# Kernel optimization log

Measured on AMD Instinct MI355X. Metric: run time of the kernel, lower is better.

## Reference

```python
import jax, jax.numpy as jnp
import numpy as np

DIM = 1024; HEADS = 16; HEAD = 64; FFN_H = 4096
LE = 8; TOPK = 2; DIM_E = 512; DIM_S = 1024
B = 1; S = 2048; N = B * S; NMOE = 2
THETA = 10000.0; EPS = 1e-6; RSF = 1.0


def rmsnorm(x, g):
    return x * jax.lax.rsqrt(jnp.mean(x * x, axis=-1, keepdims=True) + EPS) * g


def rotary(x):
    # x: [b, h, s, a]; matches RotaryEmb: split halves, y1=x1*cos+x2*sin, y2=-x1*sin+x2*cos
    a = x.shape[-1]; s = x.shape[2]
    inv_freq = (1.0 / THETA) ** (jnp.arange(0, a, 2, dtype=jnp.float32) / a)
    freqs = jnp.arange(s, dtype=jnp.float32)[:, None] * inv_freq[None, :]  # [s, a/2]
    cos, sin = jnp.cos(freqs), jnp.sin(freqs)
    x1, x2 = jnp.split(x, 2, axis=-1)
    return jnp.concatenate([x1 * cos + x2 * sin, -x1 * sin + x2 * cos], axis=-1)


def attention(x, attn_w, attn_o, doc):
    # causal + same-document masked attention (flex_attention mask_mod equivalent)
    b, s, d = x.shape
    xq, xk, xv = jnp.split(x @ attn_w, 3, axis=-1)
    def heads(t):
        return t.reshape(b, s, HEADS, HEAD).transpose(0, 2, 1, 3)
    xq, xk, xv = heads(xq), heads(xk), heads(xv)
    xq, xk = rotary(xq), rotary(xk)
    scores = jnp.einsum('bhqa,bhka->bhqk', xq, xk) / jnp.sqrt(jnp.float32(HEAD))
    q_idx = jnp.arange(s)
    mask = (q_idx[:, None] >= q_idx[None, :])[None] & (doc[:, :, None] == doc[:, None, :])
    scores = jnp.where(mask[:, None, :, :], scores, -jnp.inf)
    probs = jax.nn.softmax(scores, axis=-1)
    out = jnp.einsum('bhqk,bhka->bhqa', probs, xv)
    return out.transpose(0, 2, 1, 3).reshape(b, s, d) @ attn_o


def dense_layer(x, aw, ao, up, down, ag, fg, doc):
    xi = attention(rmsnorm(x, ag), aw, ao, doc) + x
    xf = rmsnorm(xi, fg)
    x1, x2 = jnp.split(xf @ up, 2, axis=-1)
    return (jax.nn.silu(x1) * x2) @ down + xi


def moe_layer(x, aw, ao, ag, fg, experts, tkeys, rbias, sup, sdown, idx, vals, doc):
    xi = attention(rmsnorm(x, ag), aw, ao, doc) + x
    xf = rmsnorm(xi, fg)                     # [b,s,d]
    flat = xf.reshape(-1, DIM)               # [N,d]
    # routing: base values + token-key logits + bias, sigmoid, renormalize
    tv = flat @ tkeys                        # [N,le]
    vals = vals + jnp.take_along_axis(tv, idx, axis=-1) + rbias[idx]
    sc = jax.nn.sigmoid(vals)
    sc = sc / jnp.sum(sc, axis=-1, keepdims=True) * RSF   # [N,k]
    # grouped-gemm experts (SwiGLU per expert); dense-over-experts then gather
    h1 = jnp.einsum('nd,edh->neh', flat, experts[0])
    h2 = jnp.einsum('nd,edh->neh', flat, experts[1])
    y_all = jnp.einsum('neh,edh->ned', jax.nn.silu(h1) * h2, experts[2])
    y_sel = jnp.take_along_axis(y_all, idx[:, :, None], axis=1)   # [N,k,d]
    y = jnp.sum(y_sel * sc[:, :, None], axis=1).reshape(xf.shape)
    # shared expert
    x1, x2 = jnp.split(xf @ sup, 2, axis=-1)
    y = y + (jax.nn.silu(x1) * x2) @ sdown
    return y + xi


def setup_inputs() -> dict:
    key = jax.random.key(0)
    ks = jax.random.split(key, 24)
    w = lambda k, shp: (jax.random.normal(k, shp, dtype=jnp.float32) * 0.02)
    inp = {
        'x': jax.random.normal(ks[0], (B, S, DIM), dtype=jnp.float32),
        'doc': jnp.sort(jax.random.randint(ks[1], (B, S), 0, 4), axis=-1).astype(jnp.int32),
        'indices': jax.random.randint(ks[2], (NMOE, N, TOPK), 0, LE).astype(jnp.int64),
        'values': jax.random.normal(ks[3], (NMOE, N, TOPK), dtype=jnp.float32),
        # 2 dense layers (first_k=1, last_k=1)
        'dense_attn_w': w(ks[4], (2, DIM, 3 * DIM)),
        'dense_attn_o': w(ks[5], (2, DIM, DIM)),
        'dense_ffn_up': w(ks[6], (2, DIM, 2 * FFN_H)),
        'dense_ffn_down': w(ks[7], (2, FFN_H, DIM)),
        'dense_attn_g': jnp.ones((2, DIM), dtype=jnp.float32),
        'dense_ffn_g': jnp.ones((2, DIM), dtype=jnp.float32),
        # 2 MoE layers
        'moe_attn_w': w(ks[8], (NMOE, DIM, 3 * DIM)),
        'moe_attn_o': w(ks[9], (NMOE, DIM, DIM)),
        'moe_attn_g': jnp.ones((NMOE, DIM), dtype=jnp.float32),
        'moe_ffn_g': jnp.ones((NMOE, DIM), dtype=jnp.float32),
        'moe_experts': w(ks[10], (NMOE, 3, LE, DIM, DIM_E)),
        'moe_token_keys': w(ks[11], (NMOE, DIM, LE)),
        'moe_router_bias': jnp.zeros((NMOE, LE), dtype=jnp.float32),
        'moe_shared_up': w(ks[12], (NMOE, DIM, 2 * DIM_S)),
        'moe_shared_down': w(ks[13], (NMOE, DIM_S, DIM)),
    }
    return inp


def reference(x, doc, indices, values, dense_attn_w, dense_attn_o, dense_ffn_up,
              dense_ffn_down, dense_attn_g, dense_ffn_g, moe_attn_w, moe_attn_o,
              moe_attn_g, moe_ffn_g, moe_experts, moe_token_keys, moe_router_bias,
              moe_shared_up, moe_shared_down):
    x = dense_layer(x, dense_attn_w[0], dense_attn_o[0], dense_ffn_up[0],
                    dense_ffn_down[0], dense_attn_g[0], dense_ffn_g[0], doc)
    for i in range(NMOE):
        x = moe_layer(x, moe_attn_w[i], moe_attn_o[i], moe_attn_g[i], moe_ffn_g[i],
                      moe_experts[i], moe_token_keys[i], moe_router_bias[i],
                      moe_shared_up[i], moe_shared_down[i], indices[i], values[i], doc)
    x = dense_layer(x, dense_attn_w[1], dense_attn_o[1], dense_ffn_up[1],
                    dense_ffn_down[1], dense_attn_g[1], dense_ffn_g[1], doc)
    return x
```

## Files before the change

### kernel.cpp

```cpp
#include <hip/hip_runtime.h>
#include <cmath>
#include <cstddef>
#include <cstdint>

#define DIMM   1024
#define HEADS  16
#define HEADD  64
#define FFN_H  4096
#define LE     8
#define TOPK   2
#define DIM_E  512
#define DIM_S  1024
#define NTOK   2048

typedef __bf16 bf16x8 __attribute__((ext_vector_type(8)));
typedef float  f32x4  __attribute__((ext_vector_type(4)));

union BF4 { __bf16 h[4]; uint2 u; };
union BF2 { __bf16 h[2]; uint32_t u; };

__device__ __forceinline__ void ldg_lds16(const __bf16* g, __bf16* l) {
    __builtin_amdgcn_global_load_lds(
        (const __attribute__((address_space(1))) uint32_t*)g,
        (__attribute__((address_space(3))) uint32_t*)l, 16, 0, 0);
}

__global__ __launch_bounds__(256) void rmsnorm_bf(
    const float* __restrict__ x, const float* __restrict__ g,
    __bf16* __restrict__ y)
{
    const int row = blockIdx.x;
    const int t = threadIdx.x;
    const float* xr = x + (size_t)row * DIMM;
    float4 v = *(const float4*)(xr + t * 4);
    float ss = v.x * v.x + v.y * v.y + v.z * v.z + v.w * v.w;
    #pragma unroll
    for (int off = 32; off > 0; off >>= 1) ss += __shfl_down(ss, off, 64);
    __shared__ float ws[4];
    if ((t & 63) == 0) ws[t >> 6] = ss;
    __syncthreads();
    const float tot = ws[0] + ws[1] + ws[2] + ws[3];
    const float scale = rsqrtf(tot * (1.0f / DIMM) + 1e-6f);
    const float4 gv = *(const float4*)(g + t * 4);
    BF4 o;
    o.h[0] = (__bf16)(v.x * scale * gv.x);
    o.h[1] = (__bf16)(v.y * scale * gv.y);
    o.h[2] = (__bf16)(v.z * scale * gv.z);
    o.h[3] = (__bf16)(v.w * scale * gv.w);
    *(uint2*)(y + (size_t)row * DIMM + t * 4) = o.u;
}

template <typename OutT>
__global__ __launch_bounds__(256) void gemm_bf_t(
    const __bf16* __restrict__ A, const __bf16* __restrict__ BT,
    const float* __restrict__ add, OutT* __restrict__ C,
    int M, int N, int K)
{
    __shared__ __bf16 As[128 * 32];
    __shared__ __bf16 Bs[128 * 32];
    const int t = threadIdx.x;
    const int m0 = blockIdx.y * 128, n0 = blockIdx.x * 128;
    const int lane = t & 63;
    const int wv = t >> 6;
    const int mw = (wv >> 1) * 64, nw = (wv & 1) * 64;
    const int fr = lane & 15;
    const int fk = ((lane >> 4) ^ ((fr >> 1) & 3)) * 8;
    const int r0 = t >> 2;
    const int q0l = (t & 3) * 8;
    const int q0s = ((t & 3) ^ ((t >> 3) & 3)) * 8;

    const __bf16* gA0 = A + (size_t)(m0 + r0) * K + q0s;
    const __bf16* gA1 = A + (size_t)(m0 + 64 + r0) * K + q0s;
    const __bf16* gB0 = BT + (size_t)(n0 + r0) * K + q0s;
    const __bf16* gB1 = BT + (size_t)(n0 + 64 + r0) * K + q0s;
    __bf16* lA0 = &As[r0 * 32 + q0l];
    __bf16* lA1 = &As[(64 + r0) * 32 + q0l];
    __bf16* lB0 = &Bs[r0 * 32 + q0l];
    __bf16* lB1 = &Bs[(64 + r0) * 32 + q0l];

    f32x4 acc[4][4];
    #pragma unroll
    for (int i = 0; i < 4; ++i)
        #pragma unroll
        for (int j = 0; j < 4; ++j) acc[i][j] = (f32x4){0.f, 0.f, 0.f, 0.f};

    for (int k0 = 0; k0 < K; k0 += 32) {
        __syncthreads();
        ldg_lds16(gA0 + k0, lA0);
        ldg_lds16(gA1 + k0, lA1);
        ldg_lds16(gB0 + k0, lB0);
        ldg_lds16(gB1 + k0, lB1);
        __syncthreads();
        bf16x8 af[4], bfr[4];
        #pragma unroll
        for (int i = 0; i < 4; ++i) {
            af[i]  = *(const bf16x8*)&As[(mw + i * 16 + fr) * 32 + fk];
            bfr[i] = *(const bf16x8*)&Bs[(nw + i * 16 + fr) * 32 + fk];
        }
        #pragma unroll
        for (int i = 0; i < 4; ++i)
            #pragma unroll
            for (int j = 0; j < 4; ++j)
                acc[i][j] = __builtin_amdgcn_mfma_f32_16x16x32_bf16(
                    af[i], bfr[j], acc[i][j], 0, 0, 0);
    }
    const int cn = lane & 15, cr = (lane >> 4) * 4;
    #pragma unroll
    for (int i = 0; i < 4; ++i)
        #pragma unroll
        for (int j = 0; j < 4; ++j)
            #pragma unroll
            for (int r = 0; r < 4; ++r) {
                const size_t off = (size_t)(m0 + mw + i * 16 + cr + r) * N
                                 + (n0 + nw + j * 16 + cn);
                if constexpr (__is_same(OutT, float))
                    C[off] = acc[i][j][r] + (add ? add[off] : 0.f);
                else
                    C[off] = (__bf16)acc[i][j][r];
            }
}

__global__ __launch_bounds__(256) void gemm_bf_splitk(
    const __bf16* __restrict__ A, const __bf16* __restrict__ BT,
    float* __restrict__ P, int M, int N, int K, int KS)
{
    __shared__ __bf16 As[128 * 32];
    __shared__ __bf16 Bs[128 * 32];
    const int t = threadIdx.x;
    const int m0 = blockIdx.y * 128, n0 = blockIdx.x * 128;
    const int kz0 = blockIdx.z * KS;
    const int lane = t & 63;
    const int wv = t >> 6;
    const int mw = (wv >> 1) * 64, nw = (wv & 1) * 64;
    const int fr = lane & 15;
    const int fk = ((lane >> 4) ^ ((fr >> 1) & 3)) * 8;
    const int r0 = t >> 2;
    const int q0l = (t & 3) * 8;
    const int q0s = ((t & 3) ^ ((t >> 3) & 3)) * 8;

    const __bf16* gA0 = A + (size_t)(m0 + r0) * K + q0s;
    const __bf16* gA1 = A + (size_t)(m0 + 64 + r0) * K + q0s;
    const __bf16* gB0 = BT + (size_t)(n0 + r0) * K + q0s;
    const __bf16* gB1 = BT + (size_t)(n0 + 64 + r0) * K + q0s;
    __bf16* lA0 = &As[r0 * 32 + q0l];
    __bf16* lA1 = &As[(64 + r0) * 32 + q0l];
    __bf16* lB0 = &Bs[r0 * 32 + q0l];
    __bf16* lB1 = &Bs[(64 + r0) * 32 + q0l];

    f32x4 acc[4][4];
    #pragma unroll
    for (int i = 0; i < 4; ++i)
        #pragma unroll
        for (int j = 0; j < 4; ++j) acc[i][j] = (f32x4){0.f, 0.f, 0.f, 0.f};

    for (int k0 = kz0; k0 < kz0 + KS; k0 += 32) {
        __syncthreads();
        ldg_lds16(gA0 + k0, lA0);
        ldg_lds16(gA1 + k0, lA1);
        ldg_lds16(gB0 + k0, lB0);
        ldg_lds16(gB1 + k0, lB1);
        __syncthreads();
        bf16x8 af[4], bfr[4];
        #pragma unroll
        for (int i = 0; i < 4; ++i) {
            af[i]  = *(const bf16x8*)&As[(mw + i * 16 + fr) * 32 + fk];
            bfr[i] = *(const bf16x8*)&Bs[(nw + i * 16 + fr) * 32 + fk];
        }
        #pragma unroll
        for (int i = 0; i < 4; ++i)
            #pragma unroll
            for (int j = 0; j < 4; ++j)
                acc[i][j] = __builtin_amdgcn_mfma_f32_16x16x32_bf16(
                    af[i], bfr[j], acc[i][j], 0, 0, 0);
    }
    float* Pz = P + (size_t)blockIdx.z * M * N;
    const int cn = lane & 15, cr = (lane >> 4) * 4;
    #pragma unroll
    for (int i = 0; i < 4; ++i)
        #pragma unroll
        for (int j = 0; j < 4; ++j)
            #pragma unroll
            for (int r = 0; r < 4; ++r) {
                const size_t off = (size_t)(m0 + mw + i * 16 + cr + r) * N
                                 + (n0 + nw + j * 16 + cn);
                Pz[off] = acc[i][j][r];
            }
}

__global__ __launch_bounds__(256) void gemm_glu(
    const __bf16* __restrict__ A, const __bf16* __restrict__ BT,
    const float* __restrict__ sc, __bf16* __restrict__ G,
    int M, int Nout, int K, int pairOff)
{
    __shared__ __bf16 As[128 * 32];
    __shared__ __bf16 Bs[128 * 32];
    const int t = threadIdx.x;
    const int m0 = blockIdx.y * 128;
    const int b  = blockIdx.x;
    const int lane = t & 63;
    const int wv = t >> 6;
    const int mw = (wv >> 1) * 64, nw = (wv & 1) * 64;
    const int fr = lane & 15;
    const int fk = ((lane >> 4) ^ ((fr >> 1) & 3)) * 8;
    const int r0 = t >> 2;
    const int q0l = (t & 3) * 8;
    const int q0s = ((t & 3) ^ ((t >> 3) & 3)) * 8;

    const int grow0 = b * 64 + ((r0 >> 6) ? 32 : 0) + (r0 & 31)
                    + ((r0 >> 5) & 1) * pairOff;
    const int grow1 = grow0 + 32;

    const __bf16* gA0 = A + (size_t)(m0 + r0) * K + q0s;
    const __bf16* gA1 = A + (size_t)(m0 + 64 + r0) * K + q0s;
    const __bf16* gB0 = BT + (size_t)grow0 * K + q0s;
    const __bf16* gB1 = BT + (size_t)grow1 * K + q0s;
    __bf16* lA0 = &As[r0 * 32 + q0l];
    __bf16* lA1 = &As[(64 + r0) * 32 + q0l];
    __bf16* lB0 = &Bs[r0 * 32 + q0l];
    __bf16* lB1 = &Bs[(64 + r0) * 32 + q0l];

    f32x4 acc[4][4];
    #pragma unroll
    for (int i = 0; i < 4; ++i)
        #pragma unroll
        for (int j = 0; j < 4; ++j) acc[i][j] = (f32x4){0.f, 0.f, 0.f, 0.f};

    for (int k0 = 0; k0 < K; k0 += 32) {
        __syncthreads();
        ldg_lds16(gA0 + k0, lA0);
        ldg_lds16(gA1 + k0, lA1);
        ldg_lds16(gB0 + k0, lB0);
        ldg_lds16(gB1 + k0, lB1);
        __syncthreads();
        bf16x8 af[4], bfr[4];
        #pragma unroll
        for (int i = 0; i < 4; ++i) {
            af[i]  = *(const bf16x8*)&As[(mw + i * 16 + fr) * 32 + fk];
            bfr[i] = *(const bf16x8*)&Bs[(nw + i * 16 + fr) * 32 + fk];
        }
        #pragma unroll
        for (int i = 0; i < 4; ++i)
            #pragma unroll
            for (int j = 0; j < 4; ++j)
                acc[i][j] = __builtin_amdgcn_mfma_f32_16x16x32_bf16(
                    af[i], bfr[j], acc[i][j], 0, 0, 0);
    }
    const int cn = lane & 15, cr = (lane >> 4) * 4;
    const int e = (b * 64) >> 9;
    #pragma unroll
    for (int i = 0; i < 4; ++i)
        #pragma unroll
        for (int r = 0; r < 4; ++r) {
            const int m = m0 + mw + i * 16 + cr + r;
            const float s = sc ? sc[m * LE + e] : 1.f;
            #pragma unroll
            for (int j = 0; j < 2; ++j) {
                const float h1 = acc[i][j][r];
                const float h2 = acc[i][j + 2][r];
                const float o = (h1 / (1.f + __expf(-h1))) * h2 * s;
                const int col = b * 64 + (nw >> 1) + j * 16 + cn;
                G[(size_t)m * Nout + col] = (__bf16)o;
            }
        }
}

__global__ __launch_bounds__(512, 2) void gemm_glu256(
    const __bf16* __restrict__ A, const __bf16* __restrict__ BT,
    const float* __restrict__ sc, __bf16* __restrict__ G,
    int M, int Nout, int K, int pairOff)
{
    __shared__ __bf16 As[4][256 * 32];
    __shared__ __bf16 Bs[4][256 * 32];
    const int t = threadIdx.x;
    const int m0 = blockIdx.y * 256;
    const int b  = blockIdx.x;
    const int lane = t & 63;
    const int wv = t >> 6;
    const int wr = wv >> 2, wc = wv & 3;
    const int fr = lane & 15;
    const int fk = ((lane >> 4) ^ ((fr >> 1) & 3)) * 8;

    const int r0 = t >> 2;
    const int c  = t & 3;
    const int cs = (c ^ ((r0 >> 1) & 3)) * 8;
    const int ldst = r0 * 32 + c * 8;

    const int rem0 = r0 & 63;
    const int grow0 = b * 128 + (r0 >> 6) * 32 + ((rem0 >> 4) & 1) * 16
                    + (rem0 & 15) + (rem0 >> 5) * pairOff;
    const int r1 = r0 + 128;
    const int rem1 = r1 & 63;
    const int grow1 = b * 128 + (r1 >> 6) * 32 + ((rem1 >> 4) & 1) * 16
                    + (rem1 & 15) + (rem1 >> 5) * pairOff;

    const __bf16* gA0 = A + (size_t)(m0 + r0) * K + cs;
    const __bf16* gA1 = A + (size_t)(m0 + 128 + r0) * K + cs;
    const __bf16* gB0 = BT + (size_t)grow0 * K + cs;
    const __bf16* gB1 = BT + (size_t)grow1 * K + cs;

    const int NT = K >> 5;

#define STAGE256(bi, kt) do {                                   \
        const int _k = (kt) << 5;                               \
        ldg_lds16(gA0 + _k, &As[bi][ldst]);                     \
        ldg_lds16(gA1 + _k, &As[bi][128 * 32 + ldst]);          \
        ldg_lds16(gB0 + _k, &Bs[bi][ldst]);                     \
        ldg_lds16(gB1 + _k, &Bs[bi][128 * 32 + ldst]);          \
    } while (0)

    f32x4 acc[8][4];
    #pragma unroll
    for (int i = 0; i < 8; ++i)
        #pragma unroll
        for (int j = 0; j < 4; ++j) acc[i][j] = (f32x4){0.f, 0.f, 0.f, 0.f};

    STAGE256(0, 0);
    STAGE256(1, 1);
    STAGE256(2, 2);
    asm volatile("s_waitcnt vmcnt(8)" ::: "memory");
    __builtin_amdgcn_s_barrier();
    asm volatile("" ::: "memory");

    for (int kt = 0; kt < NT; ++kt) {
        const int bi = kt & 3;
        if (kt + 3 < NT) STAGE256((kt + 3) & 3, kt + 3);

        bf16x8 af[8], bf[4];
        const __bf16* Ab = &As[bi][(wr * 128 + fr) * 32 + fk];
        #pragma unroll
        for (int i = 0; i < 8; ++i) af[i] = *(const bf16x8*)(Ab + i * 16 * 32);
        const __bf16* Bb = &Bs[bi][(wc * 64 + fr) * 32 + fk];
        #pragma unroll
        for (int j = 0; j < 4; ++j) bf[j] = *(const bf16x8*)(Bb + j * 16 * 32);

        #pragma unroll
        for (int i = 0; i < 8; ++i)
            #pragma unroll
            for (int j = 0; j < 4; ++j)
                acc[i][j] = __builtin_amdgcn_mfma_f32_16x16x32_bf16(
                    af[i], bf[j], acc[i][j], 0, 0, 0);

        if (kt < NT - 1) {
            if (kt < NT - 3)       asm volatile("s_waitcnt vmcnt(8)" ::: "memory");
            else if (kt == NT - 3) asm volatile("s_waitcnt vmcnt(4)" ::: "memory");
            else                   asm volatile("s_waitcnt vmcnt(0)" ::: "memory");
            __builtin_amdgcn_s_barrier();
            asm volatile("" ::: "memory");
        }
    }
#undef STAGE256

    const int cn = lane & 15, cr = (lane >> 4) * 4;
    const int e = b >> 2;
    #pragma unroll
    for (int i = 0; i < 8; ++i)
        #pragma unroll
        for (int r = 0; r < 4; ++r) {
            const int m = m0 + wr * 128 + i * 16 + cr + r;
            const float s = sc ? sc[m * LE + e] : 1.f;
            #pragma unroll
            for (int j = 0; j < 2; ++j) {
                const float h1 = acc[i][j][r];
                const float h2 = acc[i][j + 2][r];
                const float o = (h1 / (1.f + __expf(-h1))) * h2 * s;
                const int col = b * 128 + wc * 32 + j * 16 + cn;
                G[(size_t)m * Nout + col] = (__bf16)o;
            }
        }
}

__global__ __launch_bounds__(256) void reduce4_add(
    const float* __restrict__ P, const float* __restrict__ add,
    float* __restrict__ out, size_t MN)
{
    const size_t i = ((size_t)blockIdx.x * 256 + threadIdx.x) * 4;
    float4 s  = *(const float4*)(P + i);
    const float4 s1 = *(const float4*)(P + MN + i);
    const float4 s2 = *(const float4*)(P + 2 * MN + i);
    const float4 s3 = *(const float4*)(P + 3 * MN + i);
    const float4 a  = *(const float4*)(add + i);
    s.x += s1.x + s2.x + s3.x + a.x;
    s.y += s1.y + s2.y + s3.y + a.y;
    s.z += s1.z + s2.z + s3.z + a.z;
    s.w += s1.w + s2.w + s3.w + a.w;
    *(float4*)(out + i) = s;
}

__global__ __launch_bounds__(256) void reduce2_add(
    const float* __restrict__ P, const float* __restrict__ add,
    float* __restrict__ out, size_t MN)
{
    const size_t i = ((size_t)blockIdx.x * 256 + threadIdx.x) * 4;
    float4 s  = *(const float4*)(P + i);
    const float4 s1 = *(const float4*)(P + MN + i);
    const float4 a  = *(const float4*)(add + i);
    s.x += s1.x + a.x;
    s.y += s1.y + a.y;
    s.z += s1.z + a.z;
    s.w += s1.w + a.w;
    *(float4*)(out + i) = s;
}

__global__ __launch_bounds__(256) void transpose_cast(
    const float* __restrict__ in, __bf16* __restrict__ out, int R, int C)
{
    __shared__ float tile[32][33];
    const int bx = blockIdx.x * 32, by = blockIdx.y * 32;
    const size_t bz = (size_t)blockIdx.z * R * C;
    const int tx = threadIdx.x & 31, ty = threadIdx.x >> 5;
    const float* ip = in + bz;
    __bf16* op = out + bz;
    #pragma unroll
    for (int i = 0; i < 4; ++i)
        tile[ty + i * 8][tx] = ip[(size_t)(by + ty + i * 8) * C + bx + tx];
    __syncthreads();
    #pragma unroll
    for (int i = 0; i < 4; ++i)
        op[(size_t)(bx + ty + i * 8) * R + by + tx] = (__bf16)tile[tx][ty + i * 8];
}

__global__ __launch_bounds__(256) void cast_w2(
    const float* __restrict__ in, __bf16* __restrict__ out)
{
    const int i = blockIdx.x * 256 + threadIdx.x;
    const int d = i >> 12, r = i & 4095;
    const int e = r >> 9, h = r & 511;
    out[i] = (__bf16)in[(size_t)e * (DIMM * DIM_E) + d * DIM_E + h];
}

__global__ __launch_bounds__(256) void rotary_kernel(float* __restrict__ qkv)
{
    const int i = blockIdx.x * 256 + threadIdx.x;
    const int s = i >> 9;
    const int rem = i & 511;
    const int h = rem >> 5;
    const int j = rem & 31;
    const float inv_freq = __expf(-(float)j * (9.210340371976184f / 32.f));
    const float f = (float)s * inv_freq;
    float sn, cs;
    sincosf(f, &sn, &cs);
    float* base = qkv + (size_t)s * 3072 + h * 64 + j;
    const float q1 = base[0], q2 = base[32];
    base[0]  = q1 * cs + q2 * sn;
    base[32] = -q1 * sn + q2 * cs;
    const float k1 = base[1024], k2 = base[1024 + 32];
    base[1024]      = k1 * cs + k2 * sn;
    base[1024 + 32] = -k1 * sn + k2 * cs;
}

#define KS_STRIDE 72
#define VT_STRIDE 72
#define PW_STRIDE 36
#define LOG2E 1.4426950408889634f

__global__ __launch_bounds__(256) void attn_mfma(
    const float* __restrict__ qkv, const int* __restrict__ doc,
    __bf16* __restrict__ out)
{
    const int h = blockIdx.x;
    const int qb = blockIdx.y;
    const int t = threadIdx.x;
    const int wv = t >> 6, lane = t & 63;
    const int l15 = lane & 15, lhi = lane >> 4;
    const int q0w = qb * 64 + wv * 16;

    __shared__ __bf16 Ks[64 * KS_STRIDE];
    __shared__ __bf16 Vt[64 * VT_STRIDE];
    __shared__ float  Pw[4][16 * PW_STRIDE];
    __shared__ int    docs[64];

    bf16x8 qf[2];
    {
        const float* qrow = qkv + (size_t)(q0w + l15) * 3072 + h * 64 + lhi * 8;
        #pragma unroll
        for (int db = 0; db < 2; ++db) {
            const float4 v0 = *(const float4*)(qrow + db * 32);
            const float4 v1 = *(const float4*)(qrow + db * 32 + 4);
            bf16x8 f;
            f[0] = (__bf16)(v0.x * 0.125f); f[1] = (__bf16)(v0.y * 0.125f);
            f[2] = (__bf16)(v0.z * 0.125f); f[3] = (__bf16)(v0.w * 0.125f);
            f[4] = (__bf16)(v1.x * 0.125f); f[5] = (__bf16)(v1.y * 0.125f);
            f[6] = (__bf16)(v1.z * 0.125f); f[7] = (__bf16)(v1.w * 0.125f);
            qf[db] = f;
        }
    }
    int myDoc[4];
    #pragma unroll
    for (int rg = 0; rg < 4; ++rg) myDoc[rg] = doc[q0w + lhi * 4 + rg];

    float mrow[4] = {-INFINITY, -INFINITY, -INFINITY, -INFINITY};
    float lrow[4] = {0.f, 0.f, 0.f, 0.f};
    f32x4 oacc[4];
    #pragma unroll
    for (int nb = 0; nb < 4; ++nb) oacc[nb] = (f32x4){0.f, 0.f, 0.f, 0.f};

    const int docQ0 = doc[qb * 64];
    const int ntiles = qb + 1;

    for (int kt = 0; kt < ntiles; ++kt) {
        if (doc[kt * 64 + 63] < docQ0) continue;
        __syncthreads();
        {
            const int key = t >> 2, dof = (t & 3) * 16;
            const float* kr = qkv + (size_t)(kt * 64 + key) * 3072 + 1024 + h * 64 + dof;
            float kv[16];
            *(float4*)&kv[0]  = *(const float4*)(kr + 0);
            *(float4*)&kv[4]  = *(const float4*)(kr + 4);
            *(float4*)&kv[8]  = *(const float4*)(kr + 8);
            *(float4*)&kv[12] = *(const float4*)(kr + 12);
            bf16x8 p0, p1;
            #pragma unroll
            for (int j = 0; j < 8; ++j) { p0[j] = (__bf16)kv[j]; p1[j] = (__bf16)kv[8 + j]; }
            *(bf16x8*)&Ks[key * KS_STRIDE + dof] = p0;
            *(bf16x8*)&Ks[key * KS_STRIDE + dof + 8] = p1;
            const int k2 = (t & 31) * 2, df = (t >> 5) * 8;
            const float* vr0 = qkv + (size_t)(kt * 64 + k2) * 3072 + 2048 + h * 64 + df;
            float va[8], vb[8];
            *(float4*)&va[0] = *(const float4*)(vr0 + 0);
            *(float4*)&va[4] = *(const float4*)(vr0 + 4);
            *(float4*)&vb[0] = *(const float4*)(vr0 + 3072);
            *(float4*)&vb[4] = *(const float4*)(vr0 + 3076);
            #pragma unroll
            for (int d = 0; d < 8; ++d) {
                BF2 wpk;
                wpk.h[0] = (__bf16)va[d];
                wpk.h[1] = (__bf16)vb[d];
                *(uint32_t*)&Vt[(df + d) * VT_STRIDE + k2] = wpk.u;
            }
            if (t < 64) docs[t] = doc[kt * 64 + t];
        }
        __syncthreads();

        #pragma unroll
        for (int g = 0; g < 2; ++g) {
            f32x4 s[2];
            #pragma unroll
            for (int sg = 0; sg < 2; ++sg) {
                const int keyloc = g * 32 + sg * 16;
                const bf16x8 kf0 = *(const bf16x8*)&Ks[(keyloc + l15) * KS_STRIDE + lhi * 8];
                const bf16x8 kf1 = *(const bf16x8*)&Ks[(keyloc + l15) * KS_STRIDE + 32 + lhi * 8];
                f32x4 a = (f32x4){0.f, 0.f, 0.f, 0.f};
                a = __builtin_amdgcn_mfma_f32_16x16x32_bf16(qf[0], kf0, a, 0, 0, 0);
                a = __builtin_amdgcn_mfma_f32_16x16x32_bf16(qf[1], kf1, a, 0, 0, 0);
                s[sg] = a;
            }
            float sv0[4], sv1[4], cmax[4];
            #pragma unroll
            for (int rg = 0; rg < 4; ++rg) {
                const int r = q0w + lhi * 4 + rg;
                const int key0 = kt * 64 + g * 32 + l15;
                const bool v0 = (key0 <= r) && (docs[g * 32 + l15] == myDoc[rg]);
                const bool v1 = (key0 + 16 <= r) && (docs[g * 32 + 16 + l15] == myDoc[rg]);
                sv0[rg] = v0 ? s[0][rg] : -INFINITY;
                sv1[rg] = v1 ? s[1][rg] : -INFINITY;
                cmax[rg] = fmaxf(sv0[rg], sv1[rg]);
            }
            #pragma unroll
            for (int off = 1; off < 16; off <<= 1)
                #pragma unroll
                for (int rg = 0; rg < 4; ++rg)
                    cmax[rg] = fmaxf(cmax[rg], __shfl_xor(cmax[rg], off, 64));
            float alpha[4], p0[4], p1[4], rsum[4];
            #pragma unroll
            for (int rg = 0; rg < 4; ++rg) {
                const float mn = fmaxf(mrow[rg], cmax[rg]);
                alpha[rg] = (mn == -INFINITY) ? 1.f : exp2f((mrow[rg] - mn) * LOG2E);
                p0[rg] = (sv0[rg] == -INFINITY) ? 0.f : exp2f((sv0[rg] - mn) * LOG2E);
                p1[rg] = (sv1[rg] == -INFINITY) ? 0.f : exp2f((sv1[rg] - mn) * LOG2E);
                rsum[rg] = p0[rg] + p1[rg];
                mrow[rg] = mn;
            }
            #pragma unroll
            for (int off = 1; off < 16; off <<= 1)
                #pragma unroll
                for (int rg = 0; rg < 4; ++rg)
                    rsum[rg] += __shfl_xor(rsum[rg], off, 64);
            #pragma unroll
            for (int rg = 0; rg < 4; ++rg)
                lrow[rg] = lrow[rg] * alpha[rg] + rsum[rg];
            #pragma unroll
            for (int nb = 0; nb < 4; ++nb)
                #pragma unroll
                for (int rg = 0; rg < 4; ++rg)
                    oacc[nb][rg] *= alpha[rg];
            float* pp = &Pw[wv][0];
            #pragma unroll
            for (int rg = 0; rg < 4; ++rg) {
                pp[(lhi * 4 + rg) * PW_STRIDE + l15] = p0[rg];
                pp[(lhi * 4 + rg) * PW_STRIDE + 16 + l15] = p1[rg];
            }
            const f32x4 pa = *(const f32x4*)&pp[l15 * PW_STRIDE + lhi * 8];
            const f32x4 pb = *(const f32x4*)&pp[l15 * PW_STRIDE + lhi * 8 + 4];
            bf16x8 pf;
            pf[0] = (__bf16)pa[0]; pf[1] = (__bf16)pa[1];
            pf[2] = (__bf16)pa[2]; pf[3] = (__bf16)pa[3];
            pf[4] = (__bf16)pb[0]; pf[5] = (__bf16)pb[1];
            pf[6] = (__bf16)pb[2]; pf[7] = (__bf16)pb[3];
            #pragma unroll
            for (int nb = 0; nb < 4; ++nb) {
                const bf16x8 vf = *(const bf16x8*)&Vt[(nb * 16 + l15) * VT_STRIDE + g * 32 + lhi * 8];
                oacc[nb] = __builtin_amdgcn_mfma_f32_16x16x32_bf16(pf, vf, oacc[nb], 0, 0, 0);
            }
        }
    }
    float inv[4];
    #pragma unroll
    for (int rg = 0; rg < 4; ++rg) inv[rg] = 1.f / lrow[rg];
    #pragma unroll
    for (int nb = 0; nb < 4; ++nb)
        #pragma unroll
        for (int rg = 0; rg < 4; ++rg)
            out[(size_t)(q0w + lhi * 4 + rg) * DIMM + h * 64 + nb * 16 + l15] =
                (__bf16)(oacc[nb][rg] * inv[rg]);
}

__global__ __launch_bounds__(64) void router_bf(
    const __bf16* __restrict__ xf, const float* __restrict__ tkeys,
    const float* __restrict__ rbias, const int* __restrict__ idx,
    const float* __restrict__ vals, float* __restrict__ sc)
{
    const int n = blockIdx.x;
    const int t = threadIdx.x;
    const int e0 = idx[n * 2 + 0], e1 = idx[n * 2 + 1];
    float a0 = 0.f, a1 = 0.f;
    for (int d = t; d < DIMM; d += 64) {
        const float xv = (float)xf[(size_t)n * DIMM + d];
        a0 += xv * tkeys[d * LE + e0];
        a1 += xv * tkeys[d * LE + e1];
    }
    #pragma unroll
    for (int off = 32; off > 0; off >>= 1) {
        a0 += __shfl_down(a0, off, 64);
        a1 += __shfl_down(a1, off, 64);
    }
    if (t == 0) {
        const float v0 = vals[n * 2 + 0] + a0 + rbias[e0];
        const float v1 = vals[n * 2 + 1] + a1 + rbias[e1];
        const float s0 = 1.f / (1.f + __expf(-v0));
        const float s1 = 1.f / (1.f + __expf(-v1));
        const float inv = 1.f / (s0 + s1);
        float r[LE];
        #pragma unroll
        for (int e = 0; e < LE; ++e) r[e] = 0.f;
        r[e0] += s0 * inv;
        r[e1] += s1 * inv;
        #pragma unroll
        for (int e = 0; e < LE; ++e) sc[n * LE + e] = r[e];
    }
}

struct Scratch {
    float *qkv, *xi, *t1, *sc, *xA, *xB, *part;
    __bf16 *xn_bf, *attnO_bf, *xf_bf, *wbuf, *gact_bf, *gs_bf;
};

static void attn_block(const float* x_in, const __bf16* awT, const __bf16* aoT,
                       const float* ag, const int* doc, Scratch& w, hipStream_t s)
{
    rmsnorm_bf<<<NTOK, 256, 0, s>>>(x_in, ag, w.xn_bf);
    gemm_bf_t<float><<<dim3(24, 16), 256, 0, s>>>(w.xn_bf, awT, nullptr, w.qkv, NTOK, 3072, 1024);
    rotary_kernel<<<(NTOK * 512) / 256, 256, 0, s>>>(w.qkv);
    attn_mfma<<<dim3(HEADS, NTOK / 64), 256, 0, s>>>(w.qkv, doc, w.attnO_bf);
    gemm_bf_splitk<<<dim3(8, 16, 2), 256, 0, s>>>(w.attnO_bf, aoT, w.qkv, NTOK, 1024, 1024, 512);
    reduce2_add<<<(NTOK * 1024) / 1024, 256, 0, s>>>(w.qkv, x_in, w.xi, (size_t)NTOK * 1024);
}

static void dense_layer_run(const float* x_in, float* x_out,
                            const float* aw, const float* ao,
                            const float* up, const float* down,
                            const float* ag, const float* fg,
                            const int* doc, Scratch& w, hipStream_t s)
{
    __bf16* awT = w.wbuf;
    __bf16* aoT = w.wbuf + 3145728;
    __bf16* upT = w.wbuf + 4194304;
    __bf16* dnT = w.wbuf + 12582912;
    transpose_cast<<<dim3(96, 32, 1), 256, 0, s>>>(aw, awT, 1024, 3072);
    transpose_cast<<<dim3(32, 32, 1), 256, 0, s>>>(ao, aoT, 1024, 1024);
    transpose_cast<<<dim3(256, 32, 1), 256, 0, s>>>(up, upT, 1024, 8192);
    transpose_cast<<<dim3(32, 128, 1), 256, 0, s>>>(down, dnT, 4096, 1024);
    attn_block(x_in, awT, aoT, ag, doc, w, s);
    rmsnorm_bf<<<NTOK, 256, 0, s>>>(w.xi, fg, w.xf_bf);
    gemm_glu256<<<dim3(32, 8), 512, 0, s>>>(w.xf_bf, upT, nullptr, w.gact_bf, NTOK, 4096, 1024, 4096);
    gemm_bf_splitk<<<dim3(8, 16, 4), 256, 0, s>>>(w.gact_bf, dnT, w.part, NTOK, 1024, 4096, 1024);
    reduce4_add<<<(NTOK * 1024) / 1024, 256, 0, s>>>(w.part, w.xi, x_out, (size_t)NTOK * 1024);
}

static void moe_layer_run(const float* x_in, float* x_out,
                          const float* aw, const float* ao,
                          const float* ag, const float* fg,
                          const float* experts, const float* tkeys,
                          const float* rbias, const float* sup,
                          const float* sdn, const int* idx, const float* vals,
                          const int* doc, Scratch& w, hipStream_t s)
{
    __bf16* awT  = w.wbuf;
    __bf16* aoT  = w.wbuf + 3145728;
    __bf16* w01T = w.wbuf + 4194304;
    __bf16* w2c  = w.wbuf + 12582912;
    __bf16* supT = w.wbuf + 16777216;
    __bf16* sdnT = w.wbuf + 18874368;
    const size_t EW = (size_t)LE * DIMM * DIM_E;
    transpose_cast<<<dim3(96, 32, 1), 256, 0, s>>>(aw, awT, 1024, 3072);
    transpose_cast<<<dim3(32, 32, 1), 256, 0, s>>>(ao, aoT, 1024, 1024);
    transpose_cast<<<dim3(16, 32, 8), 256, 0, s>>>(experts, w01T, 1024, 512);
    transpose_cast<<<dim3(16, 32, 8), 256, 0, s>>>(experts + EW, w01T + 4194304, 1024, 512);
    cast_w2<<<16384, 256, 0, s>>>(experts + 2 * EW, w2c);
    transpose_cast<<<dim3(64, 32, 1), 256, 0, s>>>(sup, supT, 1024, 2048);
    transpose_cast<<<dim3(32, 32, 1), 256, 0, s>>>(sdn, sdnT, 1024, 1024);

    attn_block(x_in, awT, aoT, ag, doc, w, s);
    rmsnorm_bf<<<NTOK, 256, 0, s>>>(w.xi, fg, w.xf_bf);
    router_bf<<<NTOK, 64, 0, s>>>(w.xf_bf, tkeys, rbias, idx, vals, w.sc);
    gemm_glu256<<<dim3(32, 8), 512, 0, s>>>(w.xf_bf, w01T, w.sc, w.gact_bf, NTOK, 4096, 1024, 4096);
    gemm_glu<<<dim3(16, 16), 256, 0, s>>>(w.xf_bf, supT, nullptr, w.gs_bf, NTOK, 1024, 1024, 1024);
    gemm_bf_splitk<<<dim3(8, 16, 2), 256, 0, s>>>(w.gs_bf, sdnT, w.part, NTOK, 1024, 1024, 512);
    reduce2_add<<<(NTOK * 1024) / 1024, 256, 0, s>>>(w.part, w.xi, w.t1, (size_t)NTOK * 1024);
    gemm_bf_splitk<<<dim3(8, 16, 4), 256, 0, s>>>(w.gact_bf, w2c, w.part, NTOK, 1024, 4096, 1024);
    reduce4_add<<<(NTOK * 1024) / 1024, 256, 0, s>>>(w.part, w.t1, x_out, (size_t)NTOK * 1024);
}

extern "C" void kernel_launch(void* const* d_in, const int* in_sizes, int n_in,
                              void* d_out, int out_size, void* d_ws, size_t ws_size,
                              hipStream_t stream)
{
    (void)in_sizes; (void)n_in; (void)out_size; (void)ws_size;
    const float* x       = (const float*)d_in[0];
    const int*   doc     = (const int*)d_in[1];
    const int*   indices = (const int*)d_in[2];
    const float* values  = (const float*)d_in[3];
    const float* d_aw    = (const float*)d_in[4];
    const float* d_ao    = (const float*)d_in[5];
    const float* d_up    = (const float*)d_in[6];
    const float* d_down  = (const float*)d_in[7];
    const float* d_ag    = (const float*)d_in[8];
    const float* d_fg    = (const float*)d_in[9];
    const float* m_aw    = (const float*)d_in[10];
    const float* m_ao    = (const float*)d_in[11];
    const float* m_ag    = (const float*)d_in[12];
    const float* m_fg    = (const float*)d_in[13];
    const float* m_ex    = (const float*)d_in[14];
    const float* m_tk    = (const float*)d_in[15];
    const float* m_rb    = (const float*)d_in[16];
    const float* m_sup   = (const float*)d_in[17];
    const float* m_sdn   = (const float*)d_in[18];

    Scratch w;
    float* f = (float*)d_ws;
    w.qkv = f; f += 6291456;
    w.xi  = f; f += 2097152;
    float* h12 = f; f += 16777216;
    w.t1  = h12 + 8388608;
    w.sc  = f; f += 16384;
    w.xA  = f; f += 2097152;
    w.xB  = f; f += 2097152;
    __bf16* b = (__bf16*)f;
    w.xn_bf    = b; b += 2097152;
    w.attnO_bf = b; b += 2097152;
    w.xf_bf    = b; b += 2097152;
    w.wbuf     = b; b += 19922944;
    w.gact_bf  = (__bf16*)w.qkv;
    w.gs_bf    = (__bf16*)w.qkv + 8388608;
    w.part     = h12;

    float* out = (float*)d_out;

    dense_layer_run(x, w.xA, d_aw, d_ao, d_up, d_down, d_ag, d_fg, doc, w, stream);
    const size_t EXL = (size_t)3 * LE * DIMM * DIM_E;
    moe_layer_run(w.xA, w.xB,
                  m_aw, m_ao, m_ag, m_fg,
                  m_ex, m_tk, m_rb, m_sup, m_sdn,
                  indices, values, doc, w, stream);
    moe_layer_run(w.xB, w.xA,
                  m_aw + (size_t)DIMM * 3 * DIMM, m_ao + (size_t)DIMM * DIMM,
                  m_ag + DIMM, m_fg + DIMM,
                  m_ex + EXL, m_tk + DIMM * LE, m_rb + LE,
                  m_sup + (size_t)DIMM * 2 * DIM_S, m_sdn + (size_t)DIM_S * DIMM,
                  indices + (size_t)NTOK * TOPK, values + (size_t)NTOK * TOPK,
                  doc, w, stream);
    dense_layer_run(w.xA, out,
                    d_aw + (size_t)DIMM * 3 * DIMM, d_ao + (size_t)DIMM * DIMM,
                    d_up + (size_t)DIMM * 2 * FFN_H, d_down + (size_t)FFN_H * DIMM,
                    d_ag + DIMM, d_fg + DIMM, doc, w, stream);
}
```

Before: 1.296 ms.

## Fuse rotary and q-scaling into QKV GEMM epilogue with bf16 output

The QKV projection GEMM now applies rotary embedding and the 1/sqrt(d) query scaling in its epilogue and writes bf16 instead of fp32, which removes the separate rotary kernel. The attention kernel reads bf16 Q/K/V directly, loads K tiles into LDS asynchronously with an XOR swizzle instead of converting fp32 in registers, and drops the padded K stride. This targets the fp32 round trips and an extra kernel launch, at the cost of computing sincos in the GEMM epilogue and rounding Q/K/V to bf16 slightly earlier.

```diff
diff --git a/kernel.cpp b/kernel.cpp
--- a/kernel.cpp
+++ b/kernel.cpp
@@ -120,6 +120,94 @@
             }
 }
 
+__global__ __launch_bounds__(256) void gemm_qkv_rot(
+    const __bf16* __restrict__ A, const __bf16* __restrict__ BT,
+    __bf16* __restrict__ C, int M, int N, int K)
+{
+    __shared__ __bf16 As[128 * 32];
+    __shared__ __bf16 Bs[128 * 32];
+    const int t = threadIdx.x;
+    const int m0 = blockIdx.y * 128, n0 = blockIdx.x * 128;
+    const int lane = t & 63;
+    const int wv = t >> 6;
+    const int mw = (wv >> 1) * 64, nw = (wv & 1) * 64;
+    const int fr = lane & 15;
+    const int fk = ((lane >> 4) ^ ((fr >> 1) & 3)) * 8;
+    const int r0 = t >> 2;
+    const int q0l = (t & 3) * 8;
+    const int q0s = ((t & 3) ^ ((t >> 3) & 3)) * 8;
+
+    const __bf16* gA0 = A + (size_t)(m0 + r0) * K + q0s;
+    const __bf16* gA1 = A + (size_t)(m0 + 64 + r0) * K + q0s;
+    const __bf16* gB0 = BT + (size_t)(n0 + r0) * K + q0s;
+    const __bf16* gB1 = BT + (size_t)(n0 + 64 + r0) * K + q0s;
+    __bf16* lA0 = &As[r0 * 32 + q0l];
+    __bf16* lA1 = &As[(64 + r0) * 32 + q0l];
+    __bf16* lB0 = &Bs[r0 * 32 + q0l];
+    __bf16* lB1 = &Bs[(64 + r0) * 32 + q0l];
+
+    f32x4 acc[4][4];
+    #pragma unroll
+    for (int i = 0; i < 4; ++i)
+        #pragma unroll
+        for (int j = 0; j < 4; ++j) acc[i][j] = (f32x4){0.f, 0.f, 0.f, 0.f};
+
+    for (int k0 = 0; k0 < K; k0 += 32) {
+        __syncthreads();
+        ldg_lds16(gA0 + k0, lA0);
+        ldg_lds16(gA1 + k0, lA1);
+        ldg_lds16(gB0 + k0, lB0);
+        ldg_lds16(gB1 + k0, lB1);
+        __syncthreads();
+        bf16x8 af[4], bfr[4];
+        #pragma unroll
+        for (int i = 0; i < 4; ++i) {
+            af[i]  = *(const bf16x8*)&As[(mw + i * 16 + fr) * 32 + fk];
+            bfr[i] = *(const bf16x8*)&Bs[(nw + i * 16 + fr) * 32 + fk];
+        }
+        #pragma unroll
+        for (int i = 0; i < 4; ++i)
+            #pragma unroll
+            for (int j = 0; j < 4; ++j)
+                acc[i][j] = __builtin_amdgcn_mfma_f32_16x16x32_bf16(
+                    af[i], bfr[j], acc[i][j], 0, 0, 0);
+    }
+    const int cn = lane & 15, cr = (lane >> 4) * 4;
+    const int sec = n0 >> 10;
+    if (sec == 2) {
+        #pragma unroll
+        for (int i = 0; i < 4; ++i)
+            #pragma unroll
+            for (int j = 0; j < 4; ++j)
+                #pragma unroll
+                for (int r = 0; r < 4; ++r)
+                    C[(size_t)(m0 + mw + i * 16 + cr + r) * N
+                      + (n0 + nw + j * 16 + cn)] = (__bf16)acc[i][j][r];
+    } else {
+        const float qs = (sec == 0) ? 0.125f : 1.0f;
+        float invf[2];
+        #pragma unroll
+        for (int jp = 0; jp < 2; ++jp)
+            invf[jp] = __expf(-(float)(jp * 16 + cn) * 0.28782313662425572f);
+        #pragma unroll
+        for (int i = 0; i < 4; ++i)
+            #pragma unroll
+            for (int r = 0; r < 4; ++r) {
+                const int m = m0 + mw + i * 16 + cr + r;
+                #pragma unroll
+                for (int jp = 0; jp < 2; ++jp) {
+                    float sn, cs;
+                    sincosf((float)m * invf[jp], &sn, &cs);
+                    const float x1 = acc[i][jp][r];
+                    const float x2 = acc[i][jp + 2][r];
+                    const size_t off = (size_t)m * N + (n0 + nw + jp * 16 + cn);
+                    C[off]      = (__bf16)((x1 * cs + x2 * sn) * qs);
+                    C[off + 32] = (__bf16)((-x1 * sn + x2 * cs) * qs);
+                }
+            }
+    }
+}
+
 __global__ __launch_bounds__(256) void gemm_bf_splitk(
     const __bf16* __restrict__ A, const __bf16* __restrict__ BT,
     float* __restrict__ P, int M, int N, int K, int KS)
@@ -428,33 +516,12 @@
     out[i] = (__bf16)in[(size_t)e * (DIMM * DIM_E) + d * DIM_E + h];
 }
 
-__global__ __launch_bounds__(256) void rotary_kernel(float* __restrict__ qkv)
-{
-    const int i = blockIdx.x * 256 + threadIdx.x;
-    const int s = i >> 9;
-    const int rem = i & 511;
-    const int h = rem >> 5;
-    const int j = rem & 31;
-    const float inv_freq = __expf(-(float)j * (9.210340371976184f / 32.f));
-    const float f = (float)s * inv_freq;
-    float sn, cs;
-    sincosf(f, &sn, &cs);
-    float* base = qkv + (size_t)s * 3072 + h * 64 + j;
-    const float q1 = base[0], q2 = base[32];
-    base[0]  = q1 * cs + q2 * sn;
-    base[32] = -q1 * sn + q2 * cs;
-    const float k1 = base[1024], k2 = base[1024 + 32];
-    base[1024]      = k1 * cs + k2 * sn;
-    base[1024 + 32] = -k1 * sn + k2 * cs;
-}
-
-#define KS_STRIDE 72
 #define VT_STRIDE 72
 #define PW_STRIDE 36
 #define LOG2E 1.4426950408889634f
 
 __global__ __launch_bounds__(256) void attn_mfma(
-    const float* __restrict__ qkv, const int* __restrict__ doc,
+    const __bf16* __restrict__ qkv, const int* __restrict__ doc,
     __bf16* __restrict__ out)
 {
     const int h = blockIdx.x;
@@ -464,29 +531,25 @@
     const int l15 = lane & 15, lhi = lane >> 4;
     const int q0w = qb * 64 + wv * 16;
 
-    __shared__ __bf16 Ks[64 * KS_STRIDE];
+    __shared__ __bf16 Ks[64 * 64];
     __shared__ __bf16 Vt[64 * VT_STRIDE];
     __shared__ float  Pw[4][16 * PW_STRIDE];
     __shared__ int    docs[64];
 
     bf16x8 qf[2];
     {
-        const float* qrow = qkv + (size_t)(q0w + l15) * 3072 + h * 64 + lhi * 8;
-        #pragma unroll
-        for (int db = 0; db < 2; ++db) {
-            const float4 v0 = *(const float4*)(qrow + db * 32);
-            const float4 v1 = *(const float4*)(qrow + db * 32 + 4);
-            bf16x8 f;
-            f[0] = (__bf16)(v0.x * 0.125f); f[1] = (__bf16)(v0.y * 0.125f);
-            f[2] = (__bf16)(v0.z * 0.125f); f[3] = (__bf16)(v0.w * 0.125f);
-            f[4] = (__bf16)(v1.x * 0.125f); f[5] = (__bf16)(v1.y * 0.125f);
-            f[6] = (__bf16)(v1.z * 0.125f); f[7] = (__bf16)(v1.w * 0.125f);
-            qf[db] = f;
-        }
+        const __bf16* qrow = qkv + (size_t)(q0w + l15) * 3072 + h * 64 + lhi * 8;
+        qf[0] = *(const bf16x8*)(qrow);
+        qf[1] = *(const bf16x8*)(qrow + 32);
     }
     int myDoc[4];
     #pragma unroll
     for (int rg = 0; rg < 4; ++rg) myDoc[rg] = doc[q0w + lhi * 4 + rg];
+
+    const int kr0 = t >> 3;
+    const int kc  = t & 7;
+    const int cg0 = (kc ^ (kr0 & 7)) * 8;
+    const int cg1 = (kc ^ ((kr0 + 32) & 7)) * 8;
 
     float mrow[4] = {-INFINITY, -INFINITY, -INFINITY, -INFINITY};
     float lrow[4] = {0.f, 0.f, 0.f, 0.f};
@@ -501,30 +564,19 @@
         if (doc[kt * 64 + 63] < docQ0) continue;
         __syncthreads();
         {
-            const int key = t >> 2, dof = (t & 3) * 16;
-            const float* kr = qkv + (size_t)(kt * 64 + key) * 3072 + 1024 + h * 64 + dof;
-            float kv[16];
-            *(float4*)&kv[0]  = *(const float4*)(kr + 0);
-            *(float4*)&kv[4]  = *(const float4*)(kr + 4);
-            *(float4*)&kv[8]  = *(const float4*)(kr + 8);
-            *(float4*)&kv[12] = *(const float4*)(kr + 12);
-            bf16x8 p0, p1;
-            #pragma unroll
-            for (int j = 0; j < 8; ++j) { p0[j] = (__bf16)kv[j]; p1[j] = (__bf16)kv[8 + j]; }
-            *(bf16x8*)&Ks[key * KS_STRIDE + dof] = p0;
-            *(bf16x8*)&Ks[key * KS_STRIDE + dof + 8] = p1;
+            const __bf16* kbase = qkv + (size_t)(kt * 64) * 3072 + 1024 + h * 64;
+            ldg_lds16(kbase + (size_t)kr0 * 3072 + cg0, &Ks[t * 8]);
+            ldg_lds16(kbase + (size_t)(kr0 + 32) * 3072 + cg1, &Ks[2048 + t * 8]);
+
             const int k2 = (t & 31) * 2, df = (t >> 5) * 8;
-            const float* vr0 = qkv + (size_t)(kt * 64 + k2) * 3072 + 2048 + h * 64 + df;
-            float va[8], vb[8];
-            *(float4*)&va[0] = *(const float4*)(vr0 + 0);
-            *(float4*)&va[4] = *(const float4*)(vr0 + 4);
-            *(float4*)&vb[0] = *(const float4*)(vr0 + 3072);
-            *(float4*)&vb[4] = *(const float4*)(vr0 + 3076);
+            const __bf16* vr0 = qkv + (size_t)(kt * 64 + k2) * 3072 + 2048 + h * 64 + df;
+            const bf16x8 va = *(const bf16x8*)(vr0);
+            const bf16x8 vb = *(const bf16x8*)(vr0 + 3072);
             #pragma unroll
             for (int d = 0; d < 8; ++d) {
                 BF2 wpk;
-                wpk.h[0] = (__bf16)va[d];
-                wpk.h[1] = (__bf16)vb[d];
+                wpk.h[0] = va[d];
+                wpk.h[1] = vb[d];
                 *(uint32_t*)&Vt[(df + d) * VT_STRIDE + k2] = wpk.u;
             }
             if (t < 64) docs[t] = doc[kt * 64 + t];
@@ -536,9 +588,10 @@
             f32x4 s[2];
             #pragma unroll
             for (int sg = 0; sg < 2; ++sg) {
-                const int keyloc = g * 32 + sg * 16;
-                const bf16x8 kf0 = *(const bf16x8*)&Ks[(keyloc + l15) * KS_STRIDE + lhi * 8];
-                const bf16x8 kf1 = *(const bf16x8*)&Ks[(keyloc + l15) * KS_STRIDE + 32 + lhi * 8];
+                const int krow = g * 32 + sg * 16 + l15;
+                const int sw = (krow & 7);
+                const bf16x8 kf0 = *(const bf16x8*)&Ks[krow * 64 + ((lhi    ) ^ sw) * 8];
+                const bf16x8 kf1 = *(const bf16x8*)&Ks[krow * 64 + ((lhi + 4) ^ sw) * 8];
                 f32x4 a = (f32x4){0.f, 0.f, 0.f, 0.f};
                 a = __builtin_amdgcn_mfma_f32_16x16x32_bf16(qf[0], kf0, a, 0, 0, 0);
                 a = __builtin_amdgcn_mfma_f32_16x16x32_bf16(qf[1], kf1, a, 0, 0, 0);
@@ -651,16 +704,15 @@
 
 struct Scratch {
     float *qkv, *xi, *t1, *sc, *xA, *xB, *part;
-    __bf16 *xn_bf, *attnO_bf, *xf_bf, *wbuf, *gact_bf, *gs_bf;
+    __bf16 *qkvb, *xn_bf, *attnO_bf, *xf_bf, *wbuf, *gact_bf, *gs_bf;
 };
 
 static void attn_block(const float* x_in, const __bf16* awT, const __bf16* aoT,
                        const float* ag, const int* doc, Scratch& w, hipStream_t s)
 {
     rmsnorm_bf<<<NTOK, 256, 0, s>>>(x_in, ag, w.xn_bf);
-    gemm_bf_t<float><<<dim3(24, 16), 256, 0, s>>>(w.xn_bf, awT, nullptr, w.qkv, NTOK, 3072, 1024);
-    rotary_kernel<<<(NTOK * 512) / 256, 256, 0, s>>>(w.qkv);
-    attn_mfma<<<dim3(HEADS, NTOK / 64), 256, 0, s>>>(w.qkv, doc, w.attnO_bf);
+    gemm_qkv_rot<<<dim3(24, 16), 256, 0, s>>>(w.xn_bf, awT, w.qkvb, NTOK, 3072, 1024);
+    attn_mfma<<<dim3(HEADS, NTOK / 64), 256, 0, s>>>(w.qkvb, doc, w.attnO_bf);
     gemm_bf_splitk<<<dim3(8, 16, 2), 256, 0, s>>>(w.attnO_bf, aoT, w.qkv, NTOK, 1024, 1024, 512);
     reduce2_add<<<(NTOK * 1024) / 1024, 256, 0, s>>>(w.qkv, x_in, w.xi, (size_t)NTOK * 1024);
 }
@@ -759,6 +811,7 @@
     w.attnO_bf = b; b += 2097152;
     w.xf_bf    = b; b += 2097152;
     w.wbuf     = b; b += 19922944;
+    w.qkvb     = (__bf16*)w.qkv;
     w.gact_bf  = (__bf16*)w.qkv;
     w.gs_bf    = (__bf16*)w.qkv + 8388608;
     w.part     = h12;
```

Result: faster. 1.242 ms (-4.1%).
